# Kernel optimization log

Hardware: AMD Instinct MI355X
Metric: run time of the kernel (lower is better)

The kernel has to match this reference:

```python
import jax, jax.numpy as jnp
import numpy as np

N0, IN, HID, OUT, H = 262144, 128, 256, 256, 4
S1, S2, S3 = 32768, 4096, 512
E1, E2, E3 = 327680, 40960, 5120
NEG_SLOPE, BN_EPS = 0.2, 1e-5


def setup_inputs() -> dict:
    key = jax.random.key(0)
    ks = iter(jax.random.split(key, 64))
    def nrm(shape, fan_in):
        return jax.random.normal(next(ks), shape, jnp.float32) / np.sqrt(fan_in).astype(np.float32)
    inp = {"x": jax.random.normal(next(ks), (N0, IN), jnp.float32)}
    # (in_dim, full_out_dim, concat) per layer; per-head channels c = full/H if concat else full
    dims = [(IN, H * HID, True), (H * HID, H * HID, True), (H * HID, OUT, False)]
    for i, (din, dfull, concat) in enumerate(dims, 1):
        c = dfull // H if concat else dfull
        hc = H * c
        inp[f"w_src{i}"] = nrm((hc, din), din)
        inp[f"w_dst{i}"] = nrm((hc, din), din)
        inp[f"att_src{i}"] = nrm((H, c), c)
        inp[f"att_dst{i}"] = nrm((H, c), c)
        inp[f"b_conv{i}"] = jnp.zeros((dfull,), jnp.float32)
        inp[f"w_skip{i}"] = nrm((dfull, din), din)
        inp[f"b_skip{i}"] = jnp.zeros((dfull,), jnp.float32)
        inp[f"gamma{i}"] = jnp.ones((dfull,), jnp.float32)
        inp[f"beta{i}"] = jnp.zeros((dfull,), jnp.float32)
    for i, (E, nsrc, ndst) in enumerate([(E1, N0, S1), (E2, S1, S2), (E3, S2, S3)], 1):
        inp[f"edge_src{i}"] = jax.random.randint(next(ks), (E,), 0, nsrc, dtype=jnp.int32)
        inp[f"edge_dst{i}"] = jax.random.randint(next(ks), (E,), 0, ndst, dtype=jnp.int32)
    inp["size1"], inp["size2"], inp["size3"] = S1, S2, S3
    return inp


def gat_layer(x_all, size, src, dst, w_src, w_dst, a_src, a_dst, b, concat):
    c = w_src.shape[0] // H
    h_src = (x_all @ w_src.T).reshape(-1, H, c)        # [N_src,H,C]
    h_dst = (x_all[:size] @ w_dst.T).reshape(-1, H, c)  # [N_dst,H,C]
    al_src = jnp.einsum('nhc,hc->nh', h_src, a_src)
    al_dst = jnp.einsum('nhc,hc->nh', h_dst, a_dst)
    loop = jnp.arange(size, dtype=src.dtype)  # PyG add_self_loops on dst nodes
    s = jnp.concatenate([src, loop])
    d = jnp.concatenate([dst, loop])
    logits = jax.nn.leaky_relu(al_src[s] + al_dst[d], NEG_SLOPE)  # [E,H]
    m = jax.ops.segment_max(logits, d, num_segments=size)
    e = jnp.exp(logits - m[d])
    denom = jax.ops.segment_sum(e, d, num_segments=size)
    alpha = e / (denom[d] + 1e-16)
    out = jax.ops.segment_sum(h_src[s] * alpha[:, :, None], d, num_segments=size)
    out = out.reshape(size, H * c) if concat else out.mean(axis=1)
    return out + b


def batchnorm(x, g, b):
    mu = x.mean(0)
    var = x.var(0)
    return (x - mu) * jax.lax.rsqrt(var + BN_EPS) * g + b


def reference(x,
              w_src1, w_dst1, att_src1, att_dst1, b_conv1, w_skip1, b_skip1, gamma1, beta1,
              w_src2, w_dst2, att_src2, att_dst2, b_conv2, w_skip2, b_skip2, gamma2, beta2,
              w_src3, w_dst3, att_src3, att_dst3, b_conv3, w_skip3, b_skip3, gamma3, beta3,
              edge_src1, edge_dst1, edge_src2, edge_dst2, edge_src3, edge_dst3,
              size1, size2, size3):
    layers = [
        (size1, edge_src1, edge_dst1, w_src1, w_dst1, att_src1, att_dst1, b_conv1, w_skip1, b_skip1, gamma1, beta1, True),
        (size2, edge_src2, edge_dst2, w_src2, w_dst2, att_src2, att_dst2, b_conv2, w_skip2, b_skip2, gamma2, beta2, True),
        (size3, edge_src3, edge_dst3, w_src3, w_dst3, att_src3, att_dst3, b_conv3, w_skip3, b_skip3, gamma3, beta3, False),
    ]
    for (size, src, dst, ws, wd, a_s, a_d, bc, wsk, bsk, g, be, concat) in layers:
        x_t = x[:size]
        h = gat_layer(x, size, src, dst, ws, wd, a_s, a_d, bc, concat)
        h = h + x_t @ wsk.T + bsk
        h = batchnorm(h, g, be)
        x = jax.nn.elu(h)
    return x
```

## Files before the change

kernel.cpp:

```cpp
#include <hip/hip_runtime.h>
#include <math.h>

constexpr int N0 = 262144, S1 = 32768, S2 = 4096, S3 = 512;
constexpr int E1 = 327680, E2 = 40960, E3 = 5120;
constexpr float NEG = 0.2f, BN_EPS = 1e-5f;

typedef __attribute__((ext_vector_type(8))) short short8;
typedef __attribute__((ext_vector_type(4))) float f32x4;

__device__ __forceinline__ float lrelu(float x) { return x > 0.f ? x : NEG * x; }

__device__ __forceinline__ unsigned short f2b(float f) {
    unsigned int u = __float_as_uint(f);
    return (unsigned short)((u + 0x7FFFu + ((u >> 16) & 1u)) >> 16);
}
__device__ __forceinline__ float b2f(unsigned short u) {
    return __uint_as_float(((unsigned int)u) << 16);
}
__device__ __forceinline__ void ld4(const float* __restrict__ p, float* o) {
    float4 v = *(const float4*)p;
    o[0] = v.x; o[1] = v.y; o[2] = v.z; o[3] = v.w;
}

__device__ __forceinline__ void gload_lds16(const unsigned short* g, unsigned short* l) {
    __builtin_amdgcn_global_load_lds(
        (const __attribute__((address_space(1))) unsigned int*)g,
        (__attribute__((address_space(3))) unsigned int*)l, 16, 0, 0);
}

struct PrepArgs {
    const float* att[6]; const float* wf[6]; float* v[6];
    const float* csrc[6]; unsigned short* cdst[6];
    int* zptr; int zn4;
};

__global__ void prep_kernel(PrepArgs a)
{
    int b = blockIdx.x, t = threadIdx.x;
    if (b < 68) {
        int f, cb;
        if (b < 2)       { f = 0; cb = b; }
        else if (b < 4)  { f = 1; cb = b - 2; }
        else if (b < 20) { f = 2; cb = b - 4; }
        else if (b < 36) { f = 3; cb = b - 20; }
        else if (b < 52) { f = 4; cb = b - 36; }
        else             { f = 5; cb = b - 52; }
        int din = (f < 2) ? 128 : 1024;
        int idx = cb * 256 + t;
        int h = idx / din, k = idx - h * din;
        const float* ar = a.att[f] + h * 256;
        const float* wr = a.wf[f] + (size_t)(h * 256) * din + k;
        float acc = 0.f;
        for (int j = 0; j < 256; ++j) acc += ar[j] * wr[(size_t)j * din];
        a.v[f][idx] = acc;
    } else if (b < 124) {
        int c = b - 68, j, ob;
        if (c < 2)       { j = 0; ob = c; }
        else if (c < 4)  { j = 1; ob = c - 2; }
        else if (c < 20) { j = 2; ob = c - 4; }
        else if (c < 36) { j = 3; ob = c - 20; }
        else if (c < 40) { j = 4; ob = c - 36; }
        else             { j = 5; ob = c - 40; }
        long base = (long)ob * 65536;
        if (j < 5) {
            const float* src = a.csrc[j];
            unsigned short* dst = a.cdst[j];
            for (int it = 0; it < 64; ++it) {
                long e = base + (long)(it * 256 + t) * 4;
                float4 v = *(const float4*)(src + e);
                ushort4 u;
                u.x = f2b(v.x); u.y = f2b(v.y); u.z = f2b(v.z); u.w = f2b(v.w);
                *(ushort4*)(dst + e) = u;
            }
        } else {
            const float* src = a.csrc[5];
            unsigned short* dst = a.cdst[5];
            for (int it = 0; it < 64; ++it) {
                long e = base + (long)(it * 256 + t) * 4;
                int row = (int)(e >> 12);
                int hk = (int)(e & 4095);
                int h = hk >> 10, k = hk & 1023;
                float4 v = *(const float4*)(src + ((size_t)(h * 256 + row) << 10) + k);
                ushort4 u;
                u.x = f2b(0.25f * v.x); u.y = f2b(0.25f * v.y);
                u.z = f2b(0.25f * v.z); u.w = f2b(0.25f * v.w);
                *(ushort4*)(dst + e) = u;
            }
        }
    } else {
        int i = (b - 124) * 256 + t;
        if (i < a.zn4) ((int4*)a.zptr)[i] = make_int4(0, 0, 0, 0);
    }
}

struct CsrArgs {
    const int* edst[3]; const int* esrc[3];
    int* counts[3]; int* offsets[3]; int* cursor[3]; int* slist[3];
    int sizes[3];
};

__global__ void count_all(CsrArgs a)
{
    int id = blockIdx.x * 256 + threadIdx.x;
    int L, e;
    if (id < E1)           { L = 0; e = id; }
    else if (id < E1 + E2) { L = 1; e = id - E1; }
    else if (id < E1 + E2 + E3) { L = 2; e = id - E1 - E2; }
    else return;
    atomicAdd(&a.counts[L][a.edst[L][e]], 1);
}

__global__ void scan_all(CsrArgs a)
{
    __shared__ int lds[1024];
    int L = blockIdx.x;
    int size = a.sizes[L];
    const int* counts = a.counts[L];
    int* offsets = a.offsets[L];
    int* cursor = a.cursor[L];
    int t = threadIdx.x;
    int chunk = (size + 1023) >> 10;
    int begin = t * chunk;
    int end = begin + chunk; if (end > size) end = size;
    if (begin > size) begin = size;
    int s = 0;
    if ((chunk & 3) == 0) {
        for (int i = begin; i < end; i += 4) {
            int4 v = *(const int4*)(counts + i);
            s += v.x + v.y + v.z + v.w;
        }
    } else {
        for (int i = begin; i < end; ++i) s += counts[i];
    }
    lds[t] = s;
    __syncthreads();
    for (int d = 1; d < 1024; d <<= 1) {
        int v = (t >= d) ? lds[t - d] : 0;
        __syncthreads();
        lds[t] += v;
        __syncthreads();
    }
    int base = (t > 0) ? lds[t - 1] : 0;
    for (int i = begin; i < end; ++i) {
        offsets[i] = base; cursor[i] = base;
        base += counts[i];
    }
    if (t == 1023) offsets[size] = lds[1023];
}

__global__ void scatter_all(CsrArgs a)
{
    int id = blockIdx.x * 256 + threadIdx.x;
    int L, e;
    if (id < E1)           { L = 0; e = id; }
    else if (id < E1 + E2) { L = 1; e = id - E1; }
    else if (id < E1 + E2 + E3) { L = 2; e = id - E1 - E2; }
    else return;
    int p = atomicAdd(&a.cursor[L][a.edst[L][e]], 1);
    a.slist[L][p] = a.esrc[L][e];
}

__global__ void al128f_kernel(const float* __restrict__ x, const float* __restrict__ vs,
                              const float* __restrict__ vd, unsigned short* __restrict__ xb,
                              float* __restrict__ als, float* __restrict__ ald, int n, int ndst)
{
    int lane = threadIdx.x & 63;
    int wave = (blockIdx.x * 256 + threadIdx.x) >> 6;
    int nw = (gridDim.x * 256) >> 6;
    int j32 = lane & 31, half = lane >> 5;
    float vsr[4][4], vdr[4][4];
    #pragma unroll
    for (int h = 0; h < 4; ++h) {
        ld4(vs + h * 128 + j32 * 4, vsr[h]);
        ld4(vd + h * 128 + j32 * 4, vdr[h]);
    }
    for (long node = (long)wave * 2 + half; node < n; node += (long)nw * 2) {
        float4 xv = *(const float4*)(x + node * 128 + j32 * 4);
        ushort4 u;
        u.x = f2b(xv.x); u.y = f2b(xv.y); u.z = f2b(xv.z); u.w = f2b(xv.w);
        *(ushort4*)(xb + node * 128 + j32 * 4) = u;
        float xf[4] = { xv.x, xv.y, xv.z, xv.w };
        float a[4], bv[4];
        bool isd = node < ndst;
        #pragma unroll
        for (int h = 0; h < 4; ++h)
            a[h] = xf[0]*vsr[h][0] + xf[1]*vsr[h][1] + xf[2]*vsr[h][2] + xf[3]*vsr[h][3];
        if (isd) {
            #pragma unroll
            for (int h = 0; h < 4; ++h)
                bv[h] = xf[0]*vdr[h][0] + xf[1]*vdr[h][1] + xf[2]*vdr[h][2] + xf[3]*vdr[h][3];
        }
        #pragma unroll
        for (int off = 16; off > 0; off >>= 1) {
            #pragma unroll
            for (int h = 0; h < 4; ++h) a[h] += __shfl_xor(a[h], off);
            if (isd)
                #pragma unroll
                for (int h = 0; h < 4; ++h) bv[h] += __shfl_xor(bv[h], off);
        }
        if (j32 == 0) {
            *(float4*)(als + node * 4) = make_float4(a[0], a[1], a[2], a[3]);
            if (isd) *(float4*)(ald + node * 4) = make_float4(bv[0], bv[1], bv[2], bv[3]);
        }
    }
}

__global__ void al1024d_kernel(const unsigned short* __restrict__ xb,
                               const float* __restrict__ vs, const float* __restrict__ vd,
                               float* __restrict__ als, float* __restrict__ ald,
                               int nsrc, int ndst, int bsrc)
{
    bool isdst = (int)blockIdx.x >= bsrc;
    const float* v = isdst ? vd : vs;
    float* al = isdst ? ald : als;
    int n = isdst ? ndst : nsrc;
    int b0 = isdst ? blockIdx.x - bsrc : blockIdx.x;
    int nb = isdst ? gridDim.x - bsrc : bsrc;
    int lane = threadIdx.x & 63;
    int wave = (b0 * 256 + threadIdx.x) >> 6;
    int nwaves = (nb * 256) >> 6;
    float vr[4][16];
    #pragma unroll
    for (int h = 0; h < 4; ++h)
        #pragma unroll
        for (int it = 0; it < 2; ++it) {
            ld4(v + h * 1024 + it * 512 + lane * 8,     &vr[h][it * 8]);
            ld4(v + h * 1024 + it * 512 + lane * 8 + 4, &vr[h][it * 8 + 4]);
        }
    for (long node = wave; node < n; node += nwaves) {
        const unsigned short* xr = xb + node * 1024;
        float a[4] = {0.f, 0.f, 0.f, 0.f};
        #pragma unroll
        for (int it = 0; it < 2; ++it) {
            short8 u = *(const short8*)(xr + it * 512 + lane * 8);
            #pragma unroll
            for (int j = 0; j < 8; ++j) {
                float xv = b2f((unsigned short)u[j]);
                #pragma unroll
                for (int h = 0; h < 4; ++h) a[h] += xv * vr[h][it * 8 + j];
            }
        }
        #pragma unroll
        for (int off = 32; off > 0; off >>= 1)
            #pragma unroll
            for (int h = 0; h < 4; ++h) a[h] += __shfl_xor(a[h], off);
        if (lane == 0) *(float4*)(al + node * 4) = make_float4(a[0], a[1], a[2], a[3]);
    }
}

__global__ void mdnw_kernel(const float* __restrict__ als, const float* __restrict__ ald,
                            const int* __restrict__ offsets, const int* __restrict__ slist,
                            int size, float* __restrict__ aself, float* __restrict__ walpha)
{
    int d = blockIdx.x * 4 + (threadIdx.x >> 6);
    if (d >= size) return;
    int lane = threadIdx.x & 63;
    float ad[4], sl[4], q[4];
    ld4(ald + 4 * (size_t)d, ad);
    ld4(als + 4 * (size_t)d, q);
    #pragma unroll
    for (int h = 0; h < 4; ++h) sl[h] = lrelu(q[h] + ad[h]);
    int beg = offsets[d], deg = offsets[d + 1] - beg;
    float m[4] = { sl[0], sl[1], sl[2], sl[3] };
    for (int p = lane; p < deg; p += 64) {
        int s = slist[beg + p];
        ld4(als + 4 * (size_t)s, q);
        #pragma unroll
        for (int h = 0; h < 4; ++h) m[h] = fmaxf(m[h], lrelu(q[h] + ad[h]));
    }
    #pragma unroll
    for (int off = 32; off > 0; off >>= 1)
        #pragma unroll
        for (int h = 0; h < 4; ++h) m[h] = fmaxf(m[h], __shfl_xor(m[h], off));
    float dn[4] = {0.f, 0.f, 0.f, 0.f};
    for (int p = lane; p < deg; p += 64) {
        int s = slist[beg + p];
        ld4(als + 4 * (size_t)s, q);
        #pragma unroll
        for (int h = 0; h < 4; ++h) dn[h] += expf(lrelu(q[h] + ad[h]) - m[h]);
    }
    #pragma unroll
    for (int off = 32; off > 0; off >>= 1)
        #pragma unroll
        for (int h = 0; h < 4; ++h) dn[h] += __shfl_xor(dn[h], off);
    float r[4];
    #pragma unroll
    for (int h = 0; h < 4; ++h)
        r[h] = 1.f / (dn[h] + expf(sl[h] - m[h]) + 1e-16f);
    if (lane == 0) {
        float4 w;
        w.x = expf(sl[0] - m[0]) * r[0];
        w.y = expf(sl[1] - m[1]) * r[1];
        w.z = expf(sl[2] - m[2]) * r[2];
        w.w = expf(sl[3] - m[3]) * r[3];
        *(float4*)(aself + 4 * (size_t)d) = w;
    }
    for (int p = lane; p < deg; p += 64) {
        int s = slist[beg + p];
        ld4(als + 4 * (size_t)s, q);
        float4 w;
        w.x = expf(lrelu(q[0] + ad[0]) - m[0]) * r[0];
        w.y = expf(lrelu(q[1] + ad[1]) - m[1]) * r[1];
        w.z = expf(lrelu(q[2] + ad[2]) - m[2]) * r[2];
        w.w = expf(lrelu(q[3] + ad[3]) - m[3]) * r[3];
        *(float4*)(walpha + 4 * (size_t)(beg + p)) = w;
    }
}

__global__ void agg128_kernel(const unsigned short* __restrict__ xb, const float* __restrict__ walpha,
                              const float* __restrict__ aself,
                              const int* __restrict__ offsets, const int* __restrict__ slist,
                              unsigned short* __restrict__ aggb)
{
    int d = blockIdx.x, lane = threadIdx.x;
    int beg = offsets[d], end = offsets[d + 1];
    float w[4], acc[4][2];
    ld4(aself + 4 * (size_t)d, w);
    {
        unsigned int u = *(const unsigned int*)(xb + (size_t)d * 128 + lane * 2);
        float x0 = b2f((unsigned short)(u & 0xFFFF)), x1 = b2f((unsigned short)(u >> 16));
        #pragma unroll
        for (int h = 0; h < 4; ++h) { acc[h][0] = w[h] * x0; acc[h][1] = w[h] * x1; }
    }
    for (int p = beg; p < end; ++p) {
        int s = slist[p];
        ld4(walpha + 4 * (size_t)p, w);
        unsigned int u = *(const unsigned int*)(xb + (size_t)s * 128 + lane * 2);
        float x0 = b2f((unsigned short)(u & 0xFFFF)), x1 = b2f((unsigned short)(u >> 16));
        #pragma unroll
        for (int h = 0; h < 4; ++h) { acc[h][0] += w[h] * x0; acc[h][1] += w[h] * x1; }
    }
    unsigned int* og = (unsigned int*)(aggb + (size_t)d * 512);
    #pragma unroll
    for (int h = 0; h < 4; ++h)
        og[h * 64 + lane] = (unsigned int)f2b(acc[h][0]) | ((unsigned int)f2b(acc[h][1]) << 16);
}

__global__ void agg1024_kernel(const unsigned short* __restrict__ xb, const float* __restrict__ walpha,
                               const float* __restrict__ aself,
                               const int* __restrict__ offsets, const int* __restrict__ slist,
                               unsigned short* __restrict__ aggb)
{
    int d = blockIdx.x, t = threadIdx.x;
    int beg = offsets[d], end = offsets[d + 1];
    float w[4], acc[4][4];
    ld4(aself + 4 * (size_t)d, w);
    {
        ushort4 u = *(const ushort4*)(xb + (size_t)d * 1024 + t * 4);
        float xv[4] = { b2f(u.x), b2f(u.y), b2f(u.z), b2f(u.w) };
        #pragma unroll
        for (int h = 0; h < 4; ++h)
            #pragma unroll
            for (int j = 0; j < 4; ++j) acc[h][j] = w[h] * xv[j];
    }
    for (int p = beg; p < end; ++p) {
        int s = slist[p];
        ld4(walpha + 4 * (size_t)p, w);
        ushort4 u = *(const ushort4*)(xb + (size_t)s * 1024 + t * 4);
        float xv[4] = { b2f(u.x), b2f(u.y), b2f(u.z), b2f(u.w) };
        #pragma unroll
        for (int h = 0; h < 4; ++h)
            #pragma unroll
            for (int j = 0; j < 4; ++j) acc[h][j] += w[h] * xv[j];
    }
    unsigned short* og = aggb + (size_t)d * 4096;
    #pragma unroll
    for (int h = 0; h < 4; ++h) {
        ushort4 u;
        u.x = f2b(acc[h][0]); u.y = f2b(acc[h][1]);
        u.z = f2b(acc[h][2]); u.w = f2b(acc[h][3]);
        *(ushort4*)(og + h * 1024 + t * 4) = u;
    }
}

#define SWZ(r, c) ((((c) ^ (((r) >> 1) & 3)) << 3))

template<int BM, int BN>
__global__ __launch_bounds__(256) void gemm2_kernel(
    const unsigned short* __restrict__ A1, int lda1, const unsigned short* __restrict__ W1, int K1,
    const unsigned short* __restrict__ A2, int lda2, const unsigned short* __restrict__ W2, int K2,
    int hs2, int cph2,
    unsigned short* __restrict__ C, int N,
    float* __restrict__ bnsum, float* __restrict__ bnsq)
{
    constexpr int WM = BM / 2, WN = BN / 2;
    constexpr int TM = WM / 16, TN = WN / 16;
    constexpr int APASS = (BM * 4) / 256, BPASS = (BN * 4) / 256;
    __shared__ __align__(16) unsigned short As[BM * 32];
    __shared__ __align__(16) unsigned short Bs[BN * 32];
    __shared__ float sbn[2 * BN];
    int tid = threadIdx.x;
    int gx = gridDim.x;
    int nwg = gx * gridDim.y;
    int bid = blockIdx.y * gx + blockIdx.x;
    int cpx = nwg >> 3;
    int swz = (bid & 7) * cpx + (bid >> 3);
    int n0 = (swz % gx) * BN, m0 = (swz / gx) * BM;
    int l = tid & 63, l16 = l & 15, kq = l >> 4;
    int wid = tid >> 6, wr = wid >> 1, wc = wid & 1;

    f32x4 acc[TM][TN];
    #pragma unroll
    for (int mi = 0; mi < TM; ++mi)
        #pragma unroll
        for (int ni = 0; ni < TN; ++ni) acc[mi][ni] = (f32x4){0.f, 0.f, 0.f, 0.f};

    #pragma unroll
    for (int ph = 0; ph < 2; ++ph) {
        const unsigned short* Ap = ph ? A2 + (size_t)m0 * lda2 + (cph2 ? (size_t)(n0 / cph2) * hs2 : 0)
                                      : A1 + (size_t)m0 * lda1;
        int lda = ph ? lda2 : lda1;
        const unsigned short* Wp = ph ? W2 + (size_t)n0 * K2 : W1 + (size_t)n0 * K1;
        int ldw = ph ? K2 : K1;
        int K = ph ? K2 : K1;
        for (int k0 = 0; k0 < K; k0 += 32) {
            #pragma unroll
            for (int ps = 0; ps < APASS; ++ps) {
                int sbase = ps * 256 + wid * 64;
                int s = sbase + l;
                int r = s >> 2, cc = s & 3;
                gload_lds16(Ap + (size_t)r * lda + k0 + ((cc ^ ((r >> 1) & 3)) << 3),
                            &As[(size_t)sbase * 8]);
            }
            #pragma unroll
            for (int ps = 0; ps < BPASS; ++ps) {
                int sbase = ps * 256 + wid * 64;
                int s = sbase + l;
                int r = s >> 2, cc = s & 3;
                gload_lds16(Wp + (size_t)r * ldw + k0 + ((cc ^ ((r >> 1) & 3)) << 3),
                            &Bs[(size_t)sbase * 8]);
            }
            __syncthreads();
            short8 af[TM], bfr[TN];
            #pragma unroll
            for (int mi = 0; mi < TM; ++mi) {
                int r = wr * WM + mi * 16 + l16;
                af[mi] = *(const short8*)&As[r * 32 + SWZ(r, kq)];
            }
            #pragma unroll
            for (int ni = 0; ni < TN; ++ni) {
                int r = wc * WN + ni * 16 + l16;
                bfr[ni] = *(const short8*)&Bs[r * 32 + SWZ(r, kq)];
            }
            #pragma unroll
            for (int mi = 0; mi < TM; ++mi)
                #pragma unroll
                for (int ni = 0; ni < TN; ++ni)
                    acc[mi][ni] = __builtin_amdgcn_mfma_f32_16x16x32_bf16(
                        af[mi], bfr[ni], acc[mi][ni], 0, 0, 0);
            __syncthreads();
        }
    }

    if (tid < 2 * BN) sbn[tid] = 0.f;
    __syncthreads();

    #pragma unroll
    for (int ni = 0; ni < TN; ++ni) {
        int col = wc * WN + ni * 16 + l16;
        float s = 0.f, q = 0.f;
        #pragma unroll
        for (int mi = 0; mi < TM; ++mi) {
            int rowb = wr * WM + mi * 16 + (kq << 2);
            #pragma unroll
            for (int r = 0; r < 4; ++r) {
                float v = acc[mi][ni][r];
                C[(size_t)(m0 + rowb + r) * N + n0 + col] = f2b(v);
                s += v; q += v * v;
            }
        }
        atomicAdd(&sbn[col * 2 + 0], s);
        atomicAdd(&sbn[col * 2 + 1], q);
    }
    __syncthreads();
    if (tid < BN) {
        atomicAdd(&bnsum[n0 + tid], sbn[tid * 2 + 0]);
        atomicAdd(&bnsq[n0 + tid], sbn[tid * 2 + 1]);
    }
}

__global__ __launch_bounds__(256) void gemm3_splitk(
    const unsigned short* __restrict__ A1, const unsigned short* __restrict__ W1,
    const unsigned short* __restrict__ A2, const unsigned short* __restrict__ W2,
    float* __restrict__ Cpart)
{
    constexpr int BM = 64, BN = 64, WM = 32, WN = 32, TM = 2, TN = 2;
    __shared__ __align__(16) unsigned short As[BM * 32];
    __shared__ __align__(16) unsigned short Bs[BN * 32];
    int tid = threadIdx.x;
    int n0 = blockIdx.x * BN, m0 = blockIdx.y * BM;
    int z = blockIdx.z;
    int ph = (z >= 2);
    int ks = ph ? (z - 2) * 512 : z * 512;
    const unsigned short* Ap = ph ? A2 + (size_t)m0 * 4096 : A1 + (size_t)m0 * 1024;
    const unsigned short* Wp = ph ? W2 + (size_t)n0 * 4096 : W1 + (size_t)n0 * 1024;
    int lda = ph ? 4096 : 1024;
    int l = tid & 63, l16 = l & 15, kq = l >> 4;
    int wid = tid >> 6, wr = wid >> 1, wc = wid & 1;

    f32x4 acc[TM][TN];
    #pragma unroll
    for (int mi = 0; mi < TM; ++mi)
        #pragma unroll
        for (int ni = 0; ni < TN; ++ni) acc[mi][ni] = (f32x4){0.f, 0.f, 0.f, 0.f};

    for (int k0 = ks; k0 < ks + 512; k0 += 32) {
        {
            int sbase = wid * 64;
            int s = sbase + l;
            int r = s >> 2, cc = s & 3;
            gload_lds16(Ap + (size_t)r * lda + k0 + ((cc ^ ((r >> 1) & 3)) << 3),
                        &As[(size_t)sbase * 8]);
            gload_lds16(Wp + (size_t)r * lda + k0 + ((cc ^ ((r >> 1) & 3)) << 3),
                        &Bs[(size_t)sbase * 8]);
        }
        __syncthreads();
        short8 af[TM], bfr[TN];
        #pragma unroll
        for (int mi = 0; mi < TM; ++mi) {
            int r = wr * WM + mi * 16 + l16;
            af[mi] = *(const short8*)&As[r * 32 + SWZ(r, kq)];
        }
        #pragma unroll
        for (int ni = 0; ni < TN; ++ni) {
            int r = wc * WN + ni * 16 + l16;
            bfr[ni] = *(const short8*)&Bs[r * 32 + SWZ(r, kq)];
        }
        #pragma unroll
        for (int mi = 0; mi < TM; ++mi)
            #pragma unroll
            for (int ni = 0; ni < TN; ++ni)
                acc[mi][ni] = __builtin_amdgcn_mfma_f32_16x16x32_bf16(
                    af[mi], bfr[ni], acc[mi][ni], 0, 0, 0);
        __syncthreads();
    }

    float* Cz = Cpart + (size_t)z * S3 * 256;
    #pragma unroll
    for (int ni = 0; ni < TN; ++ni) {
        int col = wc * WN + ni * 16 + l16;
        #pragma unroll
        for (int mi = 0; mi < TM; ++mi) {
            int rowb = wr * WM + mi * 16 + (kq << 2);
            #pragma unroll
            for (int r = 0; r < 4; ++r)
                Cz[(size_t)(m0 + rowb + r) * 256 + n0 + col] = acc[mi][ni][r];
        }
    }
}

__global__ void bnstat3_kernel(const float* __restrict__ Cpart, float* __restrict__ hb32,
                               float* __restrict__ bnsum, float* __restrict__ bnsq)
{
    int c = threadIdx.x;
    int r0 = blockIdx.x * 64;
    float s = 0.f, q = 0.f;
    for (int r = r0; r < r0 + 64; ++r) {
        float v = 0.f;
        #pragma unroll
        for (int z = 0; z < 10; ++z)
            v += Cpart[((size_t)z * S3 + r) * 256 + c];
        hb32[(size_t)r * 256 + c] = v;
        s += v; q += v * v;
    }
    atomicAdd(&bnsum[c], s);
    atomicAdd(&bnsq[c], q);
}

__global__ void norm_elu_bb(const unsigned short* __restrict__ h,
                            const float* __restrict__ sum, const float* __restrict__ sq,
                            const float* __restrict__ gamma, const float* __restrict__ beta,
                            unsigned short* __restrict__ out, int N, float invM, long total)
{
    long i0 = ((long)blockIdx.x * 256 + threadIdx.x) * 8;
    if (i0 >= total) return;
    #pragma unroll
    for (int g = 0; g < 2; ++g) {
        long i = i0 + g * 4;
        int c = (int)(i % N);
        float4 sm = *(const float4*)(sum + c);
        float4 qq = *(const float4*)(sq + c);
        float4 gm = *(const float4*)(gamma + c);
        float4 bt = *(const float4*)(beta + c);
        float mu0 = sm.x * invM, mu1 = sm.y * invM, mu2 = sm.z * invM, mu3 = sm.w * invM;
        float sc0 = gm.x * rsqrtf(qq.x * invM - mu0 * mu0 + BN_EPS);
        float sc1 = gm.y * rsqrtf(qq.y * invM - mu1 * mu1 + BN_EPS);
        float sc2 = gm.z * rsqrtf(qq.z * invM - mu2 * mu2 + BN_EPS);
        float sc3 = gm.w * rsqrtf(qq.w * invM - mu3 * mu3 + BN_EPS);
        float sh0 = bt.x - mu0 * sc0, sh1 = bt.y - mu1 * sc1;
        float sh2 = bt.z - mu2 * sc2, sh3 = bt.w - mu3 * sc3;
        ushort4 u = *(const ushort4*)(h + i);
        float v0 = b2f(u.x) * sc0 + sh0;
        float v1 = b2f(u.y) * sc1 + sh1;
        float v2 = b2f(u.z) * sc2 + sh2;
        float v3 = b2f(u.w) * sc3 + sh3;
        v0 = v0 > 0.f ? v0 : expm1f(v0);
        v1 = v1 > 0.f ? v1 : expm1f(v1);
        v2 = v2 > 0.f ? v2 : expm1f(v2);
        v3 = v3 > 0.f ? v3 : expm1f(v3);
        ushort4 o;
        o.x = f2b(v0); o.y = f2b(v1); o.z = f2b(v2); o.w = f2b(v3);
        *(ushort4*)(out + i) = o;
    }
}

__global__ void norm_elu_ff(const float* __restrict__ h,
                            const float* __restrict__ sum, const float* __restrict__ sq,
                            const float* __restrict__ gamma, const float* __restrict__ beta,
                            float* __restrict__ out, int N, float invM, long total)
{
    long i = ((long)blockIdx.x * 256 + threadIdx.x) * 4;
    if (i >= total) return;
    int c = (int)(i % N);
    float4 sm = *(const float4*)(sum + c);
    float4 qq = *(const float4*)(sq + c);
    float4 gm = *(const float4*)(gamma + c);
    float4 bt = *(const float4*)(beta + c);
    float mu0 = sm.x * invM, mu1 = sm.y * invM, mu2 = sm.z * invM, mu3 = sm.w * invM;
    float sc0 = gm.x * rsqrtf(qq.x * invM - mu0 * mu0 + BN_EPS);
    float sc1 = gm.y * rsqrtf(qq.y * invM - mu1 * mu1 + BN_EPS);
    float sc2 = gm.z * rsqrtf(qq.z * invM - mu2 * mu2 + BN_EPS);
    float sc3 = gm.w * rsqrtf(qq.w * invM - mu3 * mu3 + BN_EPS);
    float4 hv = *(const float4*)(h + i);
    float4 o;
    o.x = hv.x * sc0 + (bt.x - mu0 * sc0);
    o.y = hv.y * sc1 + (bt.y - mu1 * sc1);
    o.z = hv.z * sc2 + (bt.z - mu2 * sc2);
    o.w = hv.w * sc3 + (bt.w - mu3 * sc3);
    o.x = o.x > 0.f ? o.x : expm1f(o.x);
    o.y = o.y > 0.f ? o.y : expm1f(o.y);
    o.z = o.z > 0.f ? o.z : expm1f(o.z);
    o.w = o.w > 0.f ? o.w : expm1f(o.w);
    *(float4*)(out + i) = o;
}

extern "C" void kernel_launch(void* const* d_in, const int* in_sizes, int n_in,
                              void* d_out, int out_size, void* d_ws, size_t ws_size,
                              hipStream_t stream)
{
    const float* x = (const float*)d_in[0];
    auto P = [&](int layer, int slot) -> const float* {
        return (const float*)d_in[1 + (layer - 1) * 9 + slot];
    };
    const int* edge_src[3] = { (const int*)d_in[28], (const int*)d_in[30], (const int*)d_in[32] };
    const int* edge_dst[3] = { (const int*)d_in[29], (const int*)d_in[31], (const int*)d_in[33] };

    char* wsb = (char*)d_ws;
    size_t off = 0;
    auto alloc = [&](size_t bytes) -> void* {
        void* p = wsb + off;
        off = (off + bytes + 255) & ~(size_t)255;
        return p;
    };
    unsigned short* xb0   = (unsigned short*)alloc((size_t)N0 * 128 * 2);
    unsigned short* x1b   = (unsigned short*)alloc((size_t)S1 * 1024 * 2);
    unsigned short* x2b   = (unsigned short*)alloc((size_t)S2 * 1024 * 2);
    unsigned short* hb    = (unsigned short*)alloc((size_t)S1 * 1024 * 2);
    unsigned short* aggb  = (unsigned short*)alloc((size_t)S2 * 4096 * 2);
    unsigned short* wskipb[3] = {
        (unsigned short*)alloc(131072 * 2),
        (unsigned short*)alloc(1048576 * 2),
        (unsigned short*)alloc(262144 * 2) };
    unsigned short* wsrcb[3] = {
        (unsigned short*)alloc(131072 * 2),
        (unsigned short*)alloc(1048576 * 2),
        (unsigned short*)alloc(1048576 * 2) };
    float* vbuf[6];
    vbuf[0] = (float*)alloc(512 * 4);
    vbuf[1] = (float*)alloc(512 * 4);
    vbuf[2] = (float*)alloc(4096 * 4);
    vbuf[3] = (float*)alloc(4096 * 4);
    vbuf[4] = (float*)alloc(4096 * 4);
    vbuf[5] = (float*)alloc(4096 * 4);
    float* als     = (float*)alloc((size_t)N0 * 4 * 4);
    float* ald     = (float*)alloc((size_t)S1 * 4 * 4);
    float* aself   = (float*)alloc((size_t)S1 * 4 * 4);
    float* walpha  = (float*)alloc((size_t)E1 * 4 * 4);
    float* Cpart   = (float*)alloc((size_t)10 * S3 * 256 * 4);
    float* hb32    = (float*)alloc((size_t)S3 * 256 * 4);
    int* offsets3[3] = { (int*)alloc((S1 + 1) * 4), (int*)alloc((S2 + 1) * 4), (int*)alloc((S3 + 1) * 4) };
    int* cursor3 [3] = { (int*)alloc(S1 * 4), (int*)alloc(S2 * 4), (int*)alloc(S3 * 4) };
    int* slist3  [3] = { (int*)alloc(E1 * 4), (int*)alloc(E2 * 4), (int*)alloc(E3 * 4) };
    int zn = S1 + S2 + S3 + 6 * 1024;
    int* zreg = (int*)alloc((size_t)zn * 4);
    int* counts[3] = { zreg, zreg + S1, zreg + S1 + S2 };
    float* bnsum[3] = { (float*)(zreg + S1 + S2 + S3),
                        (float*)(zreg + S1 + S2 + S3 + 2048),
                        (float*)(zreg + S1 + S2 + S3 + 4096) };
    float* bnsq[3]  = { bnsum[0] + 1024, bnsum[1] + 1024, bnsum[2] + 1024 };

    PrepArgs pa;
    for (int L = 0; L < 3; ++L) {
        pa.att[2 * L]     = P(L + 1, 2); pa.wf[2 * L]     = P(L + 1, 0); pa.v[2 * L]     = vbuf[2 * L];
        pa.att[2 * L + 1] = P(L + 1, 3); pa.wf[2 * L + 1] = P(L + 1, 1); pa.v[2 * L + 1] = vbuf[2 * L + 1];
    }
    pa.csrc[0] = P(1, 5); pa.cdst[0] = wskipb[0];
    pa.csrc[1] = P(1, 0); pa.cdst[1] = wsrcb[0];
    pa.csrc[2] = P(2, 5); pa.cdst[2] = wskipb[1];
    pa.csrc[3] = P(2, 0); pa.cdst[3] = wsrcb[1];
    pa.csrc[4] = P(3, 5); pa.cdst[4] = wskipb[2];
    pa.csrc[5] = P(3, 0); pa.cdst[5] = wsrcb[2];
    pa.zptr = zreg; pa.zn4 = zn / 4;
    prep_kernel<<<167, 256, 0, stream>>>(pa);

    CsrArgs ca;
    for (int L = 0; L < 3; ++L) {
        ca.edst[L] = edge_dst[L]; ca.esrc[L] = edge_src[L];
        ca.counts[L] = counts[L]; ca.offsets[L] = offsets3[L];
        ca.cursor[L] = cursor3[L]; ca.slist[L] = slist3[L];
    }
    ca.sizes[0] = S1; ca.sizes[1] = S2; ca.sizes[2] = S3;
    count_all<<<(E1 + E2 + E3) / 256, 256, 0, stream>>>(ca);
    scan_all<<<3, 1024, 0, stream>>>(ca);
    scatter_all<<<(E1 + E2 + E3) / 256, 256, 0, stream>>>(ca);

    al128f_kernel<<<2048, 256, 0, stream>>>(x, vbuf[0], vbuf[1], xb0, als, ald, N0, S1);
    mdnw_kernel<<<(S1 + 3) / 4, 256, 0, stream>>>(als, ald, offsets3[0], slist3[0], S1, aself, walpha);
    agg128_kernel<<<S1, 64, 0, stream>>>(xb0, walpha, aself, offsets3[0], slist3[0], aggb);
    gemm2_kernel<128, 128><<<dim3(1024 / 128, S1 / 128), 256, 0, stream>>>(
        xb0, 128, wskipb[0], 128,
        aggb, 512, wsrcb[0], 128, 128, 256,
        hb, 1024, bnsum[0], bnsq[0]);
    norm_elu_bb<<<(int)(((long)S1 * 1024 / 8 + 255) / 256), 256, 0, stream>>>(
        hb, bnsum[0], bnsq[0], P(1, 7), P(1, 8), x1b, 1024, 1.f / S1, (long)S1 * 1024);

    al1024d_kernel<<<576, 256, 0, stream>>>(x1b, vbuf[2], vbuf[3], als, ald, S1, S2, 512);
    mdnw_kernel<<<(S2 + 3) / 4, 256, 0, stream>>>(als, ald, offsets3[1], slist3[1], S2, aself, walpha);
    agg1024_kernel<<<S2, 256, 0, stream>>>(x1b, walpha, aself, offsets3[1], slist3[1], aggb);
    gemm2_kernel<64, 64><<<dim3(1024 / 64, S2 / 64), 256, 0, stream>>>(
        x1b, 1024, wskipb[1], 1024,
        aggb, 4096, wsrcb[1], 1024, 1024, 256,
        hb, 1024, bnsum[1], bnsq[1]);
    norm_elu_bb<<<(int)(((long)S2 * 1024 / 8 + 255) / 256), 256, 0, stream>>>(
        hb, bnsum[1], bnsq[1], P(2, 7), P(2, 8), x2b, 1024, 1.f / S2, (long)S2 * 1024);

    al1024d_kernel<<<72, 256, 0, stream>>>(x2b, vbuf[4], vbuf[5], als, ald, S2, S3, 64);
    mdnw_kernel<<<(S3 + 3) / 4, 256, 0, stream>>>(als, ald, offsets3[2], slist3[2], S3, aself, walpha);
    agg1024_kernel<<<S3, 256, 0, stream>>>(x2b, walpha, aself, offsets3[2], slist3[2], aggb);
    gemm3_splitk<<<dim3(256 / 64, S3 / 64, 10), 256, 0, stream>>>(
        x2b, wskipb[2], aggb, wsrcb[2], Cpart);
    bnstat3_kernel<<<8, 256, 0, stream>>>(Cpart, hb32, bnsum[2], bnsq[2]);
    norm_elu_ff<<<(int)(((long)S3 * 256 / 4 + 255) / 256), 256, 0, stream>>>(
        hb32, bnsum[2], bnsq[2], P(3, 7), P(3, 8), (float*)d_out, 256, 1.f / S3, (long)S3 * 256);
}
```

Before: 508.2 us.

## Fuse batchnorm+ELU with source attention logits and pack agg128 waves per block

Replaces the separate normalize/ELU pass and the combined attention-logit pass with one kernel that normalizes, applies ELU, writes the bf16 activations and computes the source attention logits in the same sweep. A small follow-up kernel computes destination logits from the already-written activations. This removes one full read of the normalized activations. The agg128 launch now packs four destination waves into each 256-thread block instead of one 64-thread block per node, and the layer-2 GEMM tile changes from 64x64 to 128x64. Each wave now keeps BN scale, shift and attention vectors in registers, which could lower occupancy, and the destination-logit kernel must run after the fused kernel, adding a serial step.

```diff
diff --git a/kernel.cpp b/kernel.cpp
--- a/kernel.cpp
+++ b/kernel.cpp
@@ -205,20 +205,74 @@
     }
 }
 
-__global__ void al1024d_kernel(const unsigned short* __restrict__ xb,
-                               const float* __restrict__ vs, const float* __restrict__ vd,
-                               float* __restrict__ als, float* __restrict__ ald,
-                               int nsrc, int ndst, int bsrc)
-{
-    bool isdst = (int)blockIdx.x >= bsrc;
-    const float* v = isdst ? vd : vs;
-    float* al = isdst ? ald : als;
-    int n = isdst ? ndst : nsrc;
-    int b0 = isdst ? blockIdx.x - bsrc : blockIdx.x;
-    int nb = isdst ? gridDim.x - bsrc : bsrc;
+__global__ void norm_al_kernel(const unsigned short* __restrict__ h,
+                               const float* __restrict__ sum, const float* __restrict__ sq,
+                               const float* __restrict__ gamma, const float* __restrict__ beta,
+                               const float* __restrict__ vs,
+                               unsigned short* __restrict__ xb, float* __restrict__ als,
+                               int M, float invM)
+{
     int lane = threadIdx.x & 63;
-    int wave = (b0 * 256 + threadIdx.x) >> 6;
-    int nwaves = (nb * 256) >> 6;
+    int wave = (blockIdx.x * 256 + threadIdx.x) >> 6;
+    int nwaves = (gridDim.x * 256) >> 6;
+    float sc[16], sh[16], vr[4][16];
+    #pragma unroll
+    for (int it = 0; it < 2; ++it) {
+        int c0 = it * 512 + lane * 8;
+        #pragma unroll
+        for (int g = 0; g < 2; ++g) {
+            float4 sm = *(const float4*)(sum + c0 + g * 4);
+            float4 qq = *(const float4*)(sq + c0 + g * 4);
+            float4 gm = *(const float4*)(gamma + c0 + g * 4);
+            float4 bt = *(const float4*)(beta + c0 + g * 4);
+            int o = it * 8 + g * 4;
+            float mu;
+            mu = sm.x * invM; sc[o+0] = gm.x * rsqrtf(qq.x * invM - mu * mu + BN_EPS); sh[o+0] = bt.x - mu * sc[o+0];
+            mu = sm.y * invM; sc[o+1] = gm.y * rsqrtf(qq.y * invM - mu * mu + BN_EPS); sh[o+1] = bt.y - mu * sc[o+1];
+            mu = sm.z * invM; sc[o+2] = gm.z * rsqrtf(qq.z * invM - mu * mu + BN_EPS); sh[o+2] = bt.z - mu * sc[o+2];
+            mu = sm.w * invM; sc[o+3] = gm.w * rsqrtf(qq.w * invM - mu * mu + BN_EPS); sh[o+3] = bt.w - mu * sc[o+3];
+        }
+    }
+    #pragma unroll
+    for (int hh = 0; hh < 4; ++hh)
+        #pragma unroll
+        for (int it = 0; it < 2; ++it) {
+            ld4(vs + hh * 1024 + it * 512 + lane * 8,     &vr[hh][it * 8]);
+            ld4(vs + hh * 1024 + it * 512 + lane * 8 + 4, &vr[hh][it * 8 + 4]);
+        }
+    for (long node = wave; node < M; node += nwaves) {
+        const unsigned short* xr = h + node * 1024;
+        float a[4] = {0.f, 0.f, 0.f, 0.f};
+        #pragma unroll
+        for (int it = 0; it < 2; ++it) {
+            short8 u = *(const short8*)(xr + it * 512 + lane * 8);
+            short8 o;
+            #pragma unroll
+            for (int j = 0; j < 8; ++j) {
+                float v = b2f((unsigned short)u[j]) * sc[it * 8 + j] + sh[it * 8 + j];
+                v = v > 0.f ? v : expm1f(v);
+                unsigned short vb = f2b(v);
+                o[j] = (short)vb;
+                float xv = b2f(vb);
+                #pragma unroll
+                for (int hh = 0; hh < 4; ++hh) a[hh] += xv * vr[hh][it * 8 + j];
+            }
+            *(short8*)(xb + node * 1024 + it * 512 + lane * 8) = o;
+        }
+        #pragma unroll
+        for (int off = 32; off > 0; off >>= 1)
+            #pragma unroll
+            for (int hh = 0; hh < 4; ++hh) a[hh] += __shfl_xor(a[hh], off);
+        if (lane == 0) *(float4*)(als + node * 4) = make_float4(a[0], a[1], a[2], a[3]);
+    }
+}
+
+__global__ void al1024s_kernel(const unsigned short* __restrict__ xb, const float* __restrict__ v,
+                               float* __restrict__ al, int n)
+{
+    int lane = threadIdx.x & 63;
+    int wave = (blockIdx.x * 256 + threadIdx.x) >> 6;
+    int nwaves = (gridDim.x * 256) >> 6;
     float vr[4][16];
     #pragma unroll
     for (int h = 0; h < 4; ++h)
@@ -310,9 +364,11 @@
 __global__ void agg128_kernel(const unsigned short* __restrict__ xb, const float* __restrict__ walpha,
                               const float* __restrict__ aself,
                               const int* __restrict__ offsets, const int* __restrict__ slist,
-                              unsigned short* __restrict__ aggb)
-{
-    int d = blockIdx.x, lane = threadIdx.x;
+                              int size, unsigned short* __restrict__ aggb)
+{
+    int d = blockIdx.x * 4 + (threadIdx.x >> 6);
+    if (d >= size) return;
+    int lane = threadIdx.x & 63;
     int beg = offsets[d], end = offsets[d + 1];
     float w[4], acc[4][2];
     ld4(aself + 4 * (size_t)d, w);
@@ -565,43 +621,6 @@
     }
     atomicAdd(&bnsum[c], s);
     atomicAdd(&bnsq[c], q);
-}
-
-__global__ void norm_elu_bb(const unsigned short* __restrict__ h,
-                            const float* __restrict__ sum, const float* __restrict__ sq,
-                            const float* __restrict__ gamma, const float* __restrict__ beta,
-                            unsigned short* __restrict__ out, int N, float invM, long total)
-{
-    long i0 = ((long)blockIdx.x * 256 + threadIdx.x) * 8;
-    if (i0 >= total) return;
-    #pragma unroll
-    for (int g = 0; g < 2; ++g) {
-        long i = i0 + g * 4;
-        int c = (int)(i % N);
-        float4 sm = *(const float4*)(sum + c);
-        float4 qq = *(const float4*)(sq + c);
-        float4 gm = *(const float4*)(gamma + c);
-        float4 bt = *(const float4*)(beta + c);
-        float mu0 = sm.x * invM, mu1 = sm.y * invM, mu2 = sm.z * invM, mu3 = sm.w * invM;
-        float sc0 = gm.x * rsqrtf(qq.x * invM - mu0 * mu0 + BN_EPS);
-        float sc1 = gm.y * rsqrtf(qq.y * invM - mu1 * mu1 + BN_EPS);
-        float sc2 = gm.z * rsqrtf(qq.z * invM - mu2 * mu2 + BN_EPS);
-        float sc3 = gm.w * rsqrtf(qq.w * invM - mu3 * mu3 + BN_EPS);
-        float sh0 = bt.x - mu0 * sc0, sh1 = bt.y - mu1 * sc1;
-        float sh2 = bt.z - mu2 * sc2, sh3 = bt.w - mu3 * sc3;
-        ushort4 u = *(const ushort4*)(h + i);
-        float v0 = b2f(u.x) * sc0 + sh0;
-        float v1 = b2f(u.y) * sc1 + sh1;
-        float v2 = b2f(u.z) * sc2 + sh2;
-        float v3 = b2f(u.w) * sc3 + sh3;
-        v0 = v0 > 0.f ? v0 : expm1f(v0);
-        v1 = v1 > 0.f ? v1 : expm1f(v1);
-        v2 = v2 > 0.f ? v2 : expm1f(v2);
-        v3 = v3 > 0.f ? v3 : expm1f(v3);
-        ushort4 o;
-        o.x = f2b(v0); o.y = f2b(v1); o.z = f2b(v2); o.w = f2b(v3);
-        *(ushort4*)(out + i) = o;
-    }
 }
 
 __global__ void norm_elu_ff(const float* __restrict__ h,
@@ -716,25 +735,25 @@
 
     al128f_kernel<<<2048, 256, 0, stream>>>(x, vbuf[0], vbuf[1], xb0, als, ald, N0, S1);
     mdnw_kernel<<<(S1 + 3) / 4, 256, 0, stream>>>(als, ald, offsets3[0], slist3[0], S1, aself, walpha);
-    agg128_kernel<<<S1, 64, 0, stream>>>(xb0, walpha, aself, offsets3[0], slist3[0], aggb);
+    agg128_kernel<<<(S1 + 3) / 4, 256, 0, stream>>>(xb0, walpha, aself, offsets3[0], slist3[0], S1, aggb);
     gemm2_kernel<128, 128><<<dim3(1024 / 128, S1 / 128), 256, 0, stream>>>(
         xb0, 128, wskipb[0], 128,
         aggb, 512, wsrcb[0], 128, 128, 256,
         hb, 1024, bnsum[0], bnsq[0]);
-    norm_elu_bb<<<(int)(((long)S1 * 1024 / 8 + 255) / 256), 256, 0, stream>>>(
-        hb, bnsum[0], bnsq[0], P(1, 7), P(1, 8), x1b, 1024, 1.f / S1, (long)S1 * 1024);
-
-    al1024d_kernel<<<576, 256, 0, stream>>>(x1b, vbuf[2], vbuf[3], als, ald, S1, S2, 512);
+    norm_al_kernel<<<512, 256, 0, stream>>>(hb, bnsum[0], bnsq[0], P(1, 7), P(1, 8),
+                                            vbuf[2], x1b, als, S1, 1.f / S1);
+    al1024s_kernel<<<64, 256, 0, stream>>>(x1b, vbuf[3], ald, S2);
+
     mdnw_kernel<<<(S2 + 3) / 4, 256, 0, stream>>>(als, ald, offsets3[1], slist3[1], S2, aself, walpha);
     agg1024_kernel<<<S2, 256, 0, stream>>>(x1b, walpha, aself, offsets3[1], slist3[1], aggb);
-    gemm2_kernel<64, 64><<<dim3(1024 / 64, S2 / 64), 256, 0, stream>>>(
+    gemm2_kernel<128, 64><<<dim3(1024 / 64, S2 / 128), 256, 0, stream>>>(
         x1b, 1024, wskipb[1], 1024,
         aggb, 4096, wsrcb[1], 1024, 1024, 256,
         hb, 1024, bnsum[1], bnsq[1]);
-    norm_elu_bb<<<(int)(((long)S2 * 1024 / 8 + 255) / 256), 256, 0, stream>>>(
-        hb, bnsum[1], bnsq[1], P(2, 7), P(2, 8), x2b, 1024, 1.f / S2, (long)S2 * 1024);
-
-    al1024d_kernel<<<72, 256, 0, stream>>>(x2b, vbuf[4], vbuf[5], als, ald, S2, S3, 64);
+    norm_al_kernel<<<64, 256, 0, stream>>>(hb, bnsum[1], bnsq[1], P(2, 7), P(2, 8),
+                                           vbuf[4], x2b, als, S2, 1.f / S2);
+    al1024s_kernel<<<8, 256, 0, stream>>>(x2b, vbuf[5], ald, S3);
+
     mdnw_kernel<<<(S3 + 3) / 4, 256, 0, stream>>>(als, ald, offsets3[2], slist3[2], S3, aself, walpha);
     agg1024_kernel<<<S3, 256, 0, stream>>>(x2b, walpha, aself, offsets3[2], slist3[2], aggb);
     gemm3_splitk<<<dim3(256 / 64, S3 / 64, 10), 256, 0, stream>>>(
```

After: 573.3 us. 12.8% more time.
